# Kernel tuning notes

Measured on AMD Instinct MI355X. Metric: run time of the kernel, lower is better.

Reference implementation:

```python
import jax, jax.numpy as jnp
import numpy as np

SRC_K = 11  # source neighborhood
GUI_K = 5   # guide neighborhood


def _unfold(x, k):
    # torch F.unfold(x, k, padding=k//2).view(B, C, k*k, H, W)
    # conv_general_dilated_patches (NCHW default) stacks patches channel-major:
    # output channels ordered (C, kh, kw), matching torch's view.
    p = jax.lax.conv_general_dilated_patches(x, (k, k), (1, 1), 'SAME')
    B, _, H, W = p.shape
    C = x.shape[1]
    return p.reshape(B, C, k * k, H, W)


def _conv1x1(x, w, b):
    # w: (Cout, Cin), 1x1 conv == per-pixel linear
    return jnp.einsum('oi,bihw->bohw', w, x) + b[None, :, None, None]


def setup_inputs() -> dict:
    key = jax.random.key(0)
    ks = jax.random.split(key, 6)
    B, C, H, W = 2, 64, 112, 112
    s1 = 1.0 / np.sqrt(C).astype(np.float32)
    s3 = 1.0 / np.sqrt(2 * C).astype(np.float32)
    return {
        'f_guide': jax.random.normal(ks[0], (B, C, H, W), jnp.float32),
        'f_source': jax.random.normal(ks[1], (B, C, H, W), jnp.float32),
        'w1': jax.random.normal(ks[2], (C, C), jnp.float32) * s1,
        'b1': jnp.zeros((C,), jnp.float32),
        'w2': jax.random.normal(ks[3], (C, C), jnp.float32) * s1,
        'b2': jnp.zeros((C,), jnp.float32),
        'w3': jax.random.normal(ks[4], (C, 2 * C), jnp.float32) * s3,
        'b3': jnp.zeros((C,), jnp.float32),
    }


def reference(f_guide, f_source, w1, b1, w2, b2, w3, b3):
    g = _conv1x1(f_guide, w1, b1)    # (B,C,H,W)
    s = _conv1x1(f_source, w2, b2)   # (B,C,H,W)

    # source -> guide: gather 11x11 source neighborhoods, score vs guide pixel
    fs = _unfold(s, SRC_K)                                   # (B,C,121,H,W)
    filt = jax.nn.softmax((fs * g[:, :, None]).sum(1), 1)    # (B,121,H,W)
    f_s2g = (fs * filt[:, None]).sum(2)                      # (B,C,H,W)

    # guide -> source: gather 5x5 guide neighborhoods, score vs source pixel
    fg = _unfold(g, GUI_K)                                   # (B,C,25,H,W)
    filt2 = jax.nn.softmax((fg * s[:, :, None]).sum(1), 1)   # (B,25,H,W)
    f_g2s = (fg * filt2[:, None]).sum(2)                     # (B,C,H,W)

    fusion = _conv1x1(jnp.concatenate([f_s2g, f_g2s], axis=1), w3, b3)
    return fusion
```

## Files before the change

### kernel.cpp

```cpp
#include <hip/hip_runtime.h>
#include <hip/hip_bf16.h>

constexpr int kH  = 112;
constexpr int kW  = 112;
constexpr int kC  = 64;
constexpr int kB  = 2;
constexpr int kHW = kH * kW;
constexpr int kNP = kB * kHW;

constexpr float kLog2e = 1.4426950408889634f;

__device__ __forceinline__ int xcd1568(int bid) { return (bid & 7) * 196 + (bid >> 3); }
__device__ __forceinline__ int xcd3136(int bid) { return (bid & 7) * 392 + (bid >> 3); }

__global__ __launch_bounds__(256, 6)
void conv_gs(const float* __restrict__ fg, const float* __restrict__ fs,
             const float* __restrict__ w1, const float* __restrict__ b1,
             const float* __restrict__ w2, const float* __restrict__ b2,
             const float* __restrict__ w3, float* __restrict__ gw,
             float* __restrict__ sw, float* __restrict__ w3t)
{
    __shared__ float wt[2][64 * 64];
    for (int idx = threadIdx.x; idx < 8192; idx += 256) {
        const int t = idx >> 12, rem = idx & 4095;
        const int c = rem >> 6, o = rem & 63;
        wt[t][c * 64 + o] = (t ? w2 : w1)[o * 64 + c];
    }
    if (blockIdx.x < 32) {
        const int idx = blockIdx.x * 256 + threadIdx.x;
        const int c = idx >> 6, o = idx & 63;
        w3t[idx] = w3[o * 128 + c];
    }
    __syncthreads();

    const int d = xcd1568(blockIdx.x);
    const int grp = threadIdx.x >> 4;
    const int i   = threadIdx.x & 15;
    const int t   = i >> 3;
    const int j   = i & 7;
    const int p   = d * 16 + grp;

    const int b   = p / kHW;
    const int rem = p - b * kHW;
    const int h   = rem / kW;
    const int w   = rem - h * kW;

    const float* src  = t ? fs : fg;
    const float* bias = t ? b2 : b1;
    const float* wts  = wt[t];

    float x[8];
#pragma unroll
    for (int cc = 0; cc < 8; ++cc)
        x[cc] = src[((size_t)(b * kC + 8 * j + cc) * kH + h) * kW + w];

    float a[8];
    {
        const float4 bb0 = *(const float4*)(bias + 8 * j);
        const float4 bb1v = *(const float4*)(bias + 8 * j + 4);
        a[0] = bb0.x; a[1] = bb0.y; a[2] = bb0.z; a[3] = bb0.w;
        a[4] = bb1v.x; a[5] = bb1v.y; a[6] = bb1v.z; a[7] = bb1v.w;
    }

    for (int c0 = 0; c0 < 64; c0 += 8) {
        const int sl = c0 >> 3;
#pragma unroll
        for (int k = 0; k < 8; ++k) {
            const float xc = __shfl(x[k], sl, 8);
            const float* wr = &wts[(c0 + k) * 64 + 8 * j];
            const float4 w0 = *(const float4*)(wr);
            const float4 w1v = *(const float4*)(wr + 4);
            a[0] = fmaf(w0.x, xc, a[0]);  a[1] = fmaf(w0.y, xc, a[1]);
            a[2] = fmaf(w0.z, xc, a[2]);  a[3] = fmaf(w0.w, xc, a[3]);
            a[4] = fmaf(w1v.x, xc, a[4]); a[5] = fmaf(w1v.y, xc, a[5]);
            a[6] = fmaf(w1v.z, xc, a[6]); a[7] = fmaf(w1v.w, xc, a[7]);
        }
    }
    float* dst = (t ? sw : gw) + (size_t)p * 64 + 8 * j;
    *(float4*)(dst)     = make_float4(a[0], a[1], a[2], a[3]);
    *(float4*)(dst + 4) = make_float4(a[4], a[5], a[6], a[7]);
}

template <int NN, int KD, int RAD, bool GUARD>
__device__ __forceinline__ void attn_phase(const float* __restrict__ base,
                                           const float qs[8], int pb, int h, int w,
                                           int t, int j, float acc[8], float& l)
{
    for (int n = t; n < NN; n += 4) {
        const int q = n / KD;
        const int r = n - q * KD;
        int off;
        bool valid = true;
        if (GUARD) {
            const int hh = h + q - RAD;
            const int ww = w + r - RAD;
            valid = ((unsigned)hh < (unsigned)kH) & ((unsigned)ww < (unsigned)kW);
            const int hc = min(max(hh, 0), kH - 1);
            const int wc = min(max(ww, 0), kW - 1);
            off = hc * kW + wc;
        } else {
            off = pb + q * kW + r - (RAD * kW + RAD);
        }
        const float* np = base + (size_t)off * 64 + 8 * j;
        float4 n0 = *(const float4*)(np);
        float4 n1 = *(const float4*)(np + 4);
        if (GUARD && !valid) {
            n0 = make_float4(0.f, 0.f, 0.f, 0.f);
            n1 = make_float4(0.f, 0.f, 0.f, 0.f);
        }
        float dd = n0.x * qs[0];
        dd = fmaf(n0.y, qs[1], dd);
        dd = fmaf(n0.z, qs[2], dd);
        dd = fmaf(n0.w, qs[3], dd);
        dd = fmaf(n1.x, qs[4], dd);
        dd = fmaf(n1.y, qs[5], dd);
        dd = fmaf(n1.z, qs[6], dd);
        dd = fmaf(n1.w, qs[7], dd);
        dd += __shfl_xor(dd, 1);
        dd += __shfl_xor(dd, 2);
        dd += __shfl_xor(dd, 4);
        const float pe = __builtin_amdgcn_exp2f(dd);
        l += pe;
        acc[0] = fmaf(pe, n0.x, acc[0]);
        acc[1] = fmaf(pe, n0.y, acc[1]);
        acc[2] = fmaf(pe, n0.z, acc[2]);
        acc[3] = fmaf(pe, n0.w, acc[3]);
        acc[4] = fmaf(pe, n1.x, acc[4]);
        acc[5] = fmaf(pe, n1.y, acc[5]);
        acc[6] = fmaf(pe, n1.z, acc[6]);
        acc[7] = fmaf(pe, n1.w, acc[7]);
    }
}

__device__ __forceinline__ void merge4(float acc[8], float& l)
{
    l += __shfl_xor(l, 8);
    l += __shfl_xor(l, 16);
#pragma unroll
    for (int k = 0; k < 8; ++k) {
        acc[k] += __shfl_xor(acc[k], 8);
        acc[k] += __shfl_xor(acc[k], 16);
    }
}

__global__ __launch_bounds__(256, 6)
void attn_fuse(const float* __restrict__ gw, const float* __restrict__ sw,
               const float* __restrict__ w3t, const float* __restrict__ b3,
               float* __restrict__ out)
{
    const int d   = xcd3136(blockIdx.x);
    const int grp = threadIdx.x >> 5;
    const int i   = threadIdx.x & 31;
    const int t   = i >> 3;
    const int j   = i & 7;
    const int p   = d * 8 + grp;

    const int b  = p / kHW;
    const int pb = p - b * kHW;
    const int h  = pb / kW;
    const int w  = pb - h * kW;

    const float* gb = gw + (size_t)b * kHW * 64;
    const float* sb = sw + (size_t)b * kHW * 64;

    float fs2g[8];
    {
        float qs[8];
        const float4 g0 = *(const float4*)(gw + (size_t)p * 64 + 8 * j);
        const float4 g1 = *(const float4*)(gw + (size_t)p * 64 + 8 * j + 4);
        qs[0] = g0.x * kLog2e; qs[1] = g0.y * kLog2e;
        qs[2] = g0.z * kLog2e; qs[3] = g0.w * kLog2e;
        qs[4] = g1.x * kLog2e; qs[5] = g1.y * kLog2e;
        qs[6] = g1.z * kLog2e; qs[7] = g1.w * kLog2e;

        float acc[8] = {0.f, 0.f, 0.f, 0.f, 0.f, 0.f, 0.f, 0.f};
        float l = 0.f;
        if (h >= 5 && h < kH - 5 && w >= 5 && w < kW - 5)
            attn_phase<121, 11, 5, false>(sb, qs, pb, h, w, t, j, acc, l);
        else
            attn_phase<121, 11, 5, true>(sb, qs, pb, h, w, t, j, acc, l);
        merge4(acc, l);
        const float inv = 1.0f / l;
#pragma unroll
        for (int k = 0; k < 8; ++k) fs2g[k] = acc[k] * inv;
    }

    float fg2s[8];
    {
        float qs[8];
        const float4 s0 = *(const float4*)(sw + (size_t)p * 64 + 8 * j);
        const float4 s1 = *(const float4*)(sw + (size_t)p * 64 + 8 * j + 4);
        qs[0] = s0.x * kLog2e; qs[1] = s0.y * kLog2e;
        qs[2] = s0.z * kLog2e; qs[3] = s0.w * kLog2e;
        qs[4] = s1.x * kLog2e; qs[5] = s1.y * kLog2e;
        qs[6] = s1.z * kLog2e; qs[7] = s1.w * kLog2e;

        float acc[8] = {0.f, 0.f, 0.f, 0.f, 0.f, 0.f, 0.f, 0.f};
        float l = 0.f;
        if (h >= 2 && h < kH - 2 && w >= 2 && w < kW - 2)
            attn_phase<25, 5, 2, false>(gb, qs, pb, h, w, t, j, acc, l);
        else
            attn_phase<25, 5, 2, true>(gb, qs, pb, h, w, t, j, acc, l);
        merge4(acc, l);
        const float inv = 1.0f / l;
#pragma unroll
        for (int k = 0; k < 8; ++k) fg2s[k] = acc[k] * inv;
    }

    float xsrc[8];
#pragma unroll
    for (int k = 0; k < 8; ++k) xsrc[k] = (t < 2) ? fs2g[k] : fg2s[k];

    float fo[8] = {0.f, 0.f, 0.f, 0.f, 0.f, 0.f, 0.f, 0.f};
    for (int m0 = 0; m0 < 32; m0 += 8) {
        const int srcl = (((t & 1) << 5) + m0) >> 3;
        const float* wrow = w3t + (size_t)(t * 32 + m0) * 64 + 8 * j;
#pragma unroll
        for (int mm = 0; mm < 8; ++mm) {
            const float xc = __shfl(xsrc[mm], srcl, 8);
            const float4 w0 = *(const float4*)(wrow + mm * 64);
            const float4 w1v = *(const float4*)(wrow + mm * 64 + 4);
            fo[0] = fmaf(w0.x, xc, fo[0]);  fo[1] = fmaf(w0.y, xc, fo[1]);
            fo[2] = fmaf(w0.z, xc, fo[2]);  fo[3] = fmaf(w0.w, xc, fo[3]);
            fo[4] = fmaf(w1v.x, xc, fo[4]); fo[5] = fmaf(w1v.y, xc, fo[5]);
            fo[6] = fmaf(w1v.z, xc, fo[6]); fo[7] = fmaf(w1v.w, xc, fo[7]);
        }
    }
#pragma unroll
    for (int k = 0; k < 8; ++k) {
        fo[k] += __shfl_xor(fo[k], 8);
        fo[k] += __shfl_xor(fo[k], 16);
    }

    const float e0 = (t & 2) ? fo[4] : fo[0];
    const float e1 = (t & 2) ? fo[5] : fo[1];
    const float e2 = (t & 2) ? fo[6] : fo[2];
    const float e3 = (t & 2) ? fo[7] : fo[3];
    const float o0 = (t & 1) ? e2 : e0;
    const float o1 = (t & 1) ? e3 : e1;
    const int c0 = 8 * j + 2 * t;
    const size_t a0 = ((size_t)(b * kC + c0) * kH + h) * kW + w;
    out[a0]       = o0 + b3[c0];
    out[a0 + kHW] = o1 + b3[c0 + 1];
}

extern "C" void kernel_launch(void* const* d_in, const int* in_sizes, int n_in,
                              void* d_out, int out_size, void* d_ws, size_t ws_size,
                              hipStream_t stream)
{
    const float* fg = (const float*)d_in[0];
    const float* fs = (const float*)d_in[1];
    const float* w1 = (const float*)d_in[2];
    const float* b1 = (const float*)d_in[3];
    const float* w2 = (const float*)d_in[4];
    const float* b2 = (const float*)d_in[5];
    const float* w3 = (const float*)d_in[6];
    const float* b3 = (const float*)d_in[7];
    float* outp = (float*)d_out;

    float* gws = (float*)d_ws;
    float* sws = gws + (size_t)kNP * 64;
    float* w3t = sws + (size_t)kNP * 64;

    conv_gs<<<1568, 256, 0, stream>>>(fg, fs, w1, b1, w2, b2, w3, gws, sws, w3t);
    attn_fuse<<<3136, 256, 0, stream>>>(gws, sws, w3t, b3, outp);
}
```

Before: 182.6 us.

## Pretranspose weights, stage conv inputs in LDS, prefetch neighbors in attention loop

Adds a small prep kernel that transposes w1, w2 and w3 once, so conv_gs can copy weights into LDS with contiguous reads instead of strided gathers. conv_gs now loads each 16-pixel input tile into padded shared memory with coalesced reads before the 1x1 conv. The attention loop software-pipelines neighbor loads one iteration ahead to hide global-memory latency. Launch bounds are also retuned (conv 6->4, attn 6->8 waves), which trades registers for occupancy and adds a third kernel launch.

```diff
diff --git a/kernel.cpp b/kernel.cpp
--- a/kernel.cpp
+++ b/kernel.cpp
@@ -13,52 +13,72 @@
 __device__ __forceinline__ int xcd1568(int bid) { return (bid & 7) * 196 + (bid >> 3); }
 __device__ __forceinline__ int xcd3136(int bid) { return (bid & 7) * 392 + (bid >> 3); }
 
-__global__ __launch_bounds__(256, 6)
+__global__ __launch_bounds__(256)
+void prep(const float* __restrict__ w1, const float* __restrict__ w2,
+          const float* __restrict__ w3, float* __restrict__ w1t,
+          float* __restrict__ w2t, float* __restrict__ w3t)
+{
+    const int idx = blockIdx.x * 256 + threadIdx.x;
+    if (idx < 4096) {
+        const int o = idx >> 6, c = idx & 63;
+        w1t[c * 64 + o] = w1[idx];
+    } else if (idx < 8192) {
+        const int r = idx - 4096;
+        const int o = r >> 6, c = r & 63;
+        w2t[c * 64 + o] = w2[r];
+    } else {
+        const int r = idx - 8192;
+        const int o = r >> 7, c = r & 127;
+        w3t[c * 64 + o] = w3[r];
+    }
+}
+
+__global__ __launch_bounds__(256, 4)
 void conv_gs(const float* __restrict__ fg, const float* __restrict__ fs,
-             const float* __restrict__ w1, const float* __restrict__ b1,
-             const float* __restrict__ w2, const float* __restrict__ b2,
-             const float* __restrict__ w3, float* __restrict__ gw,
-             float* __restrict__ sw, float* __restrict__ w3t)
-{
-    __shared__ float wt[2][64 * 64];
+             const float* __restrict__ w1t, const float* __restrict__ b1,
+             const float* __restrict__ w2t, const float* __restrict__ b2,
+             float* __restrict__ gw, float* __restrict__ sw)
+{
+    __shared__ float wt[2][4096];
+    __shared__ float xls[2][64 * 17];
+
     for (int idx = threadIdx.x; idx < 8192; idx += 256) {
         const int t = idx >> 12, rem = idx & 4095;
-        const int c = rem >> 6, o = rem & 63;
-        wt[t][c * 64 + o] = (t ? w2 : w1)[o * 64 + c];
-    }
-    if (blockIdx.x < 32) {
-        const int idx = blockIdx.x * 256 + threadIdx.x;
-        const int c = idx >> 6, o = idx & 63;
-        w3t[idx] = w3[o * 128 + c];
+        wt[t][rem] = (t ? w2t : w1t)[rem];
+    }
+
+    const int d   = xcd1568(blockIdx.x);
+    const int p0  = d * 16;
+    const int b   = p0 / kHW;
+    const int pb0 = p0 - b * kHW;
+
+    for (int idx = threadIdx.x; idx < 2048; idx += 256) {
+        const int t  = idx >> 10;
+        const int c  = (idx >> 4) & 63;
+        const int px = idx & 15;
+        xls[t][c * 17 + px] = (t ? fs : fg)[(size_t)(b * kC + c) * kHW + pb0 + px];
     }
     __syncthreads();
 
-    const int d = xcd1568(blockIdx.x);
     const int grp = threadIdx.x >> 4;
     const int i   = threadIdx.x & 15;
     const int t   = i >> 3;
     const int j   = i & 7;
-    const int p   = d * 16 + grp;
-
-    const int b   = p / kHW;
-    const int rem = p - b * kHW;
-    const int h   = rem / kW;
-    const int w   = rem - h * kW;
-
-    const float* src  = t ? fs : fg;
+    const int p   = p0 + grp;
+
+    float x[8];
+#pragma unroll
+    for (int cc = 0; cc < 8; ++cc)
+        x[cc] = xls[t][(8 * j + cc) * 17 + grp];
+
     const float* bias = t ? b2 : b1;
     const float* wts  = wt[t];
 
-    float x[8];
-#pragma unroll
-    for (int cc = 0; cc < 8; ++cc)
-        x[cc] = src[((size_t)(b * kC + 8 * j + cc) * kH + h) * kW + w];
-
     float a[8];
     {
-        const float4 bb0 = *(const float4*)(bias + 8 * j);
+        const float4 bb0  = *(const float4*)(bias + 8 * j);
         const float4 bb1v = *(const float4*)(bias + 8 * j + 4);
-        a[0] = bb0.x; a[1] = bb0.y; a[2] = bb0.z; a[3] = bb0.w;
+        a[0] = bb0.x;  a[1] = bb0.y;  a[2] = bb0.z;  a[3] = bb0.w;
         a[4] = bb1v.x; a[5] = bb1v.y; a[6] = bb1v.z; a[7] = bb1v.w;
     }
 
@@ -86,49 +106,69 @@
                                            const float qs[8], int pb, int h, int w,
                                            int t, int j, float acc[8], float& l)
 {
-    for (int n = t; n < NN; n += 4) {
-        const int q = n / KD;
-        const int r = n - q * KD;
+    const float* np;
+    bool v0 = true;
+    {
+        const int q = t / KD, r = t - q * KD;
         int off;
-        bool valid = true;
         if (GUARD) {
-            const int hh = h + q - RAD;
-            const int ww = w + r - RAD;
-            valid = ((unsigned)hh < (unsigned)kH) & ((unsigned)ww < (unsigned)kW);
-            const int hc = min(max(hh, 0), kH - 1);
-            const int wc = min(max(ww, 0), kW - 1);
-            off = hc * kW + wc;
+            const int hh = h + q - RAD, ww = w + r - RAD;
+            v0 = ((unsigned)hh < (unsigned)kH) & ((unsigned)ww < (unsigned)kW);
+            off = min(max(hh, 0), kH - 1) * kW + min(max(ww, 0), kW - 1);
         } else {
             off = pb + q * kW + r - (RAD * kW + RAD);
         }
-        const float* np = base + (size_t)off * 64 + 8 * j;
-        float4 n0 = *(const float4*)(np);
-        float4 n1 = *(const float4*)(np + 4);
-        if (GUARD && !valid) {
-            n0 = make_float4(0.f, 0.f, 0.f, 0.f);
-            n1 = make_float4(0.f, 0.f, 0.f, 0.f);
-        }
-        float dd = n0.x * qs[0];
-        dd = fmaf(n0.y, qs[1], dd);
-        dd = fmaf(n0.z, qs[2], dd);
-        dd = fmaf(n0.w, qs[3], dd);
-        dd = fmaf(n1.x, qs[4], dd);
-        dd = fmaf(n1.y, qs[5], dd);
-        dd = fmaf(n1.z, qs[6], dd);
-        dd = fmaf(n1.w, qs[7], dd);
+        np = base + (size_t)off * 64 + 8 * j;
+    }
+    float4 n0 = *(const float4*)(np);
+    float4 n1 = *(const float4*)(np + 4);
+
+    for (int n = t; n < NN; n += 4) {
+        float4 m0, m1;
+        bool v1 = true;
+        if (n + 4 < NN) {
+            const int q = (n + 4) / KD, r = (n + 4) - q * KD;
+            int off;
+            if (GUARD) {
+                const int hh = h + q - RAD, ww = w + r - RAD;
+                v1 = ((unsigned)hh < (unsigned)kH) & ((unsigned)ww < (unsigned)kW);
+                off = min(max(hh, 0), kH - 1) * kW + min(max(ww, 0), kW - 1);
+            } else {
+                off = pb + q * kW + r - (RAD * kW + RAD);
+            }
+            const float* np2 = base + (size_t)off * 64 + 8 * j;
+            m0 = *(const float4*)(np2);
+            m1 = *(const float4*)(np2 + 4);
+        }
+
+        float4 c0 = n0, c1 = n1;
+        if (GUARD && !v0) {
+            c0 = make_float4(0.f, 0.f, 0.f, 0.f);
+            c1 = make_float4(0.f, 0.f, 0.f, 0.f);
+        }
+        float dd = c0.x * qs[0];
+        dd = fmaf(c0.y, qs[1], dd);
+        dd = fmaf(c0.z, qs[2], dd);
+        dd = fmaf(c0.w, qs[3], dd);
+        dd = fmaf(c1.x, qs[4], dd);
+        dd = fmaf(c1.y, qs[5], dd);
+        dd = fmaf(c1.z, qs[6], dd);
+        dd = fmaf(c1.w, qs[7], dd);
         dd += __shfl_xor(dd, 1);
         dd += __shfl_xor(dd, 2);
         dd += __shfl_xor(dd, 4);
         const float pe = __builtin_amdgcn_exp2f(dd);
         l += pe;
-        acc[0] = fmaf(pe, n0.x, acc[0]);
-        acc[1] = fmaf(pe, n0.y, acc[1]);
-        acc[2] = fmaf(pe, n0.z, acc[2]);
-        acc[3] = fmaf(pe, n0.w, acc[3]);
-        acc[4] = fmaf(pe, n1.x, acc[4]);
-        acc[5] = fmaf(pe, n1.y, acc[5]);
-        acc[6] = fmaf(pe, n1.z, acc[6]);
-        acc[7] = fmaf(pe, n1.w, acc[7]);
+        acc[0] = fmaf(pe, c0.x, acc[0]);
+        acc[1] = fmaf(pe, c0.y, acc[1]);
+        acc[2] = fmaf(pe, c0.z, acc[2]);
+        acc[3] = fmaf(pe, c0.w, acc[3]);
+        acc[4] = fmaf(pe, c1.x, acc[4]);
+        acc[5] = fmaf(pe, c1.y, acc[5]);
+        acc[6] = fmaf(pe, c1.z, acc[6]);
+        acc[7] = fmaf(pe, c1.w, acc[7]);
+
+        n0 = m0; n1 = m1; v0 = v1;
     }
 }
 
@@ -143,7 +183,7 @@
     }
 }
 
-__global__ __launch_bounds__(256, 6)
+__global__ __launch_bounds__(256, 8)
 void attn_fuse(const float* __restrict__ gw, const float* __restrict__ sw,
                const float* __restrict__ w3t, const float* __restrict__ b3,
                float* __restrict__ out)
@@ -261,7 +301,10 @@
     float* gws = (float*)d_ws;
     float* sws = gws + (size_t)kNP * 64;
     float* w3t = sws + (size_t)kNP * 64;
-
-    conv_gs<<<1568, 256, 0, stream>>>(fg, fs, w1, b1, w2, b2, w3, gws, sws, w3t);
+    float* w1t = w3t + 128 * 64;
+    float* w2t = w1t + 64 * 64;
+
+    prep<<<64, 256, 0, stream>>>(w1, w2, w3, w1t, w2t, w3t);
+    conv_gs<<<1568, 256, 0, stream>>>(fg, fs, w1t, b1, w2t, b2, gws, sws);
     attn_fuse<<<3136, 256, 0, stream>>>(gws, sws, w3t, b3, outp);
 }
```

Measured after the change: 174.2 us. 4.6% less time.
